# Performance work log

Measured on AMD Instinct MI355X. Metric: run time of the kernel, lower is better.

## Reference

```python
import jax, jax.numpy as jnp
import numpy as np

N, E, IN, HID, ADIM, EDIM, H = 20000, 320000, 128, 128, 16, 16, 2


def _lin(key, out_d, in_d, scale=0.05):
    kw, kb = jax.random.split(key)
    W = jax.random.normal(kw, (out_d, in_d), jnp.float32) * scale
    b = jax.random.normal(kb, (out_d,), jnp.float32) * scale
    return W, b


def _gat_params(key):
    k = jax.random.split(key, 4)
    Wl, bl = _lin(k[0], H * HID, HID)
    Wr, br = _lin(k[1], H * HID, HID)
    We = jax.random.normal(k[2], (H * HID, EDIM), jnp.float32) * 0.05  # lin_edge, no bias
    att = jax.random.normal(k[3], (1, H, HID), jnp.float32) * 0.05
    bias = jnp.zeros((HID,), jnp.float32)  # concat=False -> out bias of size HID
    return Wl, bl, Wr, br, We, att, bias


def setup_inputs() -> dict:
    key = jax.random.key(0)
    ks = jax.random.split(key, 16)
    inp = {}
    inp['x'] = jax.random.normal(ks[0], (N, IN), jnp.float32)
    inp['edge_index'] = jax.random.randint(ks[1], (2, E), 0, N, jnp.int64 if jax.config.jax_enable_x64 else jnp.int32)
    inp['edge_attr'] = jax.random.normal(ks[2], (E, EDIM), jnp.float32)
    inp['action'] = jax.random.normal(ks[3], (N, ADIM), jnp.float32)
    inp['inp_W'], inp['inp_b'] = _lin(ks[4], HID, IN)
    for i, name in enumerate(['s1', 's2', 'sa']):
        Wl, bl, Wr, br, We, att, bias = _gat_params(ks[5 + i])
        inp[f'{name}_Wl'], inp[f'{name}_bl'] = Wl, bl
        inp[f'{name}_Wr'], inp[f'{name}_br'] = Wr, br
        inp[f'{name}_We'], inp[f'{name}_att'], inp[f'{name}_bias'] = We, att, bias
    inp['ap_W'], inp['ap_b'] = _lin(ks[8], HID, ADIM)
    inp['g_W'], inp['g_b'] = _lin(ks[9], HID, HID)
    inp['be_W'], inp['be_b'] = _lin(ks[10], HID, HID)
    inp['q1_W'], inp['q1_b'] = _lin(ks[11], HID, HID)
    inp['q2_W'], inp['q2_b'] = _lin(ks[12], 1, HID)
    return inp


def gatv2(h, src, dst, ea, Wl, bl, Wr, br, We, att, bias):
    """PyG GATv2Conv, heads=H, concat=False (mean over heads), with edge_attr."""
    n = h.shape[0]
    xl = (h @ Wl.T + bl).reshape(n, H, HID)   # source transform
    xr = (h @ Wr.T + br).reshape(n, H, HID)   # destination transform
    em = (ea @ We.T).reshape(-1, H, HID)      # [E,H,C]
    m = jax.nn.leaky_relu(xl[src] + xr[dst] + em, 0.2)   # [E,H,C]
    logit = (m * att).sum(-1)                 # [E,H]
    lmax = jax.ops.segment_max(logit, dst, num_segments=n)
    w = jnp.exp(logit - lmax[dst])
    den = jax.ops.segment_sum(w, dst, num_segments=n)
    alpha = w / den[dst]                      # segment softmax over incoming edges
    out = jax.ops.segment_sum(alpha[..., None] * xl[src], dst, num_segments=n)  # [n,H,C]
    return out.mean(axis=1) + bias


def reference(x, edge_index, edge_attr, action, inp_W, inp_b,
              s1_Wl, s1_bl, s1_Wr, s1_br, s1_We, s1_att, s1_bias,
              s2_Wl, s2_bl, s2_Wr, s2_br, s2_We, s2_att, s2_bias,
              sa_Wl, sa_bl, sa_Wr, sa_br, sa_We, sa_att, sa_bias,
              ap_W, ap_b, g_W, g_b, be_W, be_b, q1_W, q1_b, q2_W, q2_b):
    src, dst = edge_index[0], edge_index[1]
    h = jax.nn.relu(x @ inp_W.T + inp_b)
    h = jax.nn.relu(gatv2(h, src, dst, edge_attr, s1_Wl, s1_bl, s1_Wr, s1_br, s1_We, s1_att, s1_bias))
    h = jax.nn.relu(gatv2(h, src, dst, edge_attr, s2_Wl, s2_bl, s2_Wr, s2_br, s2_We, s2_att, s2_bias))
    a = jax.nn.relu(action @ ap_W.T + ap_b)
    h = (a @ g_W.T + g_b) * h + (a @ be_W.T + be_b)   # FiLM modulation
    h = jax.nn.relu(gatv2(h, src, dst, edge_attr, sa_Wl, sa_bl, sa_Wr, sa_br, sa_We, sa_att, sa_bias))
    h = jax.nn.relu(h @ q1_W.T + q1_b)
    q_node = h @ q2_W.T + q2_b                         # [N,1]
    return q_node.mean(axis=0, keepdims=True)          # [1,1]
```

## Files before the change

### kernel.cpp

```cpp
#include <hip/hip_runtime.h>
#include <hip/hip_bf16.h>


typedef __attribute__((ext_vector_type(8))) short bf16x8;
typedef __attribute__((ext_vector_type(4))) float f32x4;
typedef __attribute__((ext_vector_type(2))) float f32x2;

#define ZERO8 ((bf16x8){0, 0, 0, 0, 0, 0, 0, 0})

__device__ __forceinline__ unsigned short f2bf(float f) {
    union { float f; unsigned int i; } v; v.f = f;
    unsigned int x = v.i;
    x += 0x7fffu + ((x >> 16) & 1u);
    return (unsigned short)(x >> 16);
}
__device__ __forceinline__ unsigned char f2fp8(float f) {
    return (unsigned char)(__builtin_amdgcn_cvt_pk_fp8_f32(f, f, 0, false) & 0xFF);
}
__device__ __forceinline__ void wave_lds_fence() {
    __builtin_amdgcn_wave_barrier();
    asm volatile("s_waitcnt lgkmcnt(0)" ::: "memory");
    __builtin_amdgcn_wave_barrier();
}

#define MAXCVT 16
struct CvtDescs {
    const float* src[MAXCVT];
    unsigned short* dst[MAXCVT];
    int off4[MAXCVT + 1];
    int cnt;
    int* deg; int ndeg4;
    int* ctr; float* col;
};
__global__ __launch_bounds__(256) void cvt_many_kernel(CvtDescs d) {
    const int tid = blockIdx.x * blockDim.x + threadIdx.x;
    const int stride = gridDim.x * blockDim.x;
    const int total = d.off4[d.cnt];
    for (int i = tid; i < total; i += stride) {
        int e = 0;
        while (d.off4[e + 1] <= i) ++e;
        const int j = i - d.off4[e];
        float4 v = ((const float4*)d.src[e])[j];
        ((ushort4*)d.dst[e])[j] = make_ushort4(f2bf(v.x), f2bf(v.y), f2bf(v.z), f2bf(v.w));
    }
    for (int i = tid; i < d.ndeg4; i += stride)
        ((int4*)d.deg)[i] = make_int4(0, 0, 0, 0);
    if (tid == 0) { *d.ctr = 0; *d.col = 0.f; }
}

__global__ void hist_kernel(const int* __restrict__ dst, int* __restrict__ deg, int n) {
    int i = blockIdx.x * blockDim.x + threadIdx.x;
    if (i < n) atomicAdd(&deg[dst[i]], 1);
}

__global__ __launch_bounds__(1024) void scan_kernel(const int* __restrict__ deg,
                                                    int* __restrict__ rowp,
                                                    int* __restrict__ cur, int n) {
    __shared__ int sums[1024];
    const int t = threadIdx.x;
    const int PER = 20;
    int base = t * PER;
    int local[PER];
    int run = 0;
#pragma unroll
    for (int i = 0; i < PER; ++i) {
        int v = (base + i < n) ? deg[base + i] : 0;
        local[i] = run; run += v;
    }
    sums[t] = run; __syncthreads();
    for (int off = 1; off < 1024; off <<= 1) {
        int v = (t >= off) ? sums[t - off] : 0;
        __syncthreads();
        sums[t] += v;
        __syncthreads();
    }
    int offs = (t > 0) ? sums[t - 1] : 0;
#pragma unroll
    for (int i = 0; i < PER; ++i) {
        int idx = base + i;
        if (idx < n) { int v = offs + local[i]; rowp[idx] = v; cur[idx] = v; }
    }
    if (t == 0) rowp[n] = sums[1023];
}

__global__ void scatter_kernel(const int* __restrict__ src, const int* __restrict__ dst,
                               int* __restrict__ cur, const float4* __restrict__ ea,
                               int* __restrict__ csrs,
                               ushort4* __restrict__ eacsr, int n) {
    int i = blockIdx.x * blockDim.x + threadIdx.x;
    if (i < n) {
        int d = dst[i];
        int p = atomicAdd(&cur[d], 1);
        csrs[p] = src[i];
        const float4* er = ea + (size_t)i * 4;
        ushort4* eo = eacsr + (size_t)p * 4;
#pragma unroll
        for (int q = 0; q < 4; ++q) {
            float4 v = er[q];
            eo[q] = make_ushort4(f2bf(v.x), f2bf(v.y), f2bf(v.z), f2bf(v.w));
        }
    }
}

template <bool RELU, bool SPLIT, bool AF32>
__global__ __launch_bounds__(256) void gemm_mfma_kernel(
    const void* __restrict__ Ap, const unsigned short* __restrict__ W,
    const float* __restrict__ bias0, const float* __restrict__ bias1, int bsplit,
    unsigned short* __restrict__ Cbf, unsigned char* __restrict__ Cf8,
    int M, int N, int K) {
    __shared__ unsigned char ctile[SPLIT ? 128 * 64 : 64];
    const int t = threadIdx.x;
    const int wave = t >> 6, lane = t & 63;
    const int lo = lane & 15, quad = lane >> 4;
    const int m0 = blockIdx.y * 128 + wave * 32;
    const int n0 = blockIdx.x * 64;

    f32x4 acc[2][4];
#pragma unroll
    for (int i = 0; i < 2; ++i)
#pragma unroll
        for (int j = 0; j < 4; ++j) acc[i][j] = (f32x4){0.f, 0.f, 0.f, 0.f};

    for (int k0 = 0; k0 < K; k0 += 32) {
        bf16x8 af[2], bfr[4];
#pragma unroll
        for (int mi = 0; mi < 2; ++mi) {
            const int mb = m0 + mi * 16;
            if (mb >= M) { af[mi] = ZERO8; continue; }
            if (AF32) {
                const float* A = (const float*)Ap;
                float4 a0 = *(const float4*)(A + (size_t)(mb + lo) * K + k0 + quad * 8);
                float4 a1 = *(const float4*)(A + (size_t)(mb + lo) * K + k0 + quad * 8 + 4);
                bf16x8 f;
                f[0] = (short)f2bf(a0.x); f[1] = (short)f2bf(a0.y);
                f[2] = (short)f2bf(a0.z); f[3] = (short)f2bf(a0.w);
                f[4] = (short)f2bf(a1.x); f[5] = (short)f2bf(a1.y);
                f[6] = (short)f2bf(a1.z); f[7] = (short)f2bf(a1.w);
                af[mi] = f;
            } else {
                const unsigned short* A = (const unsigned short*)Ap;
                af[mi] = *(const bf16x8*)(A + (size_t)(mb + lo) * K + k0 + quad * 8);
            }
        }
#pragma unroll
        for (int ni = 0; ni < 4; ++ni)
            bfr[ni] = *(const bf16x8*)(W + (size_t)(n0 + ni * 16 + lo) * K + k0 + quad * 8);
#pragma unroll
        for (int mi = 0; mi < 2; ++mi)
#pragma unroll
            for (int ni = 0; ni < 4; ++ni)
                acc[mi][ni] = __builtin_amdgcn_mfma_f32_16x16x32_bf16(af[mi], bfr[ni], acc[mi][ni], 0, 0, 0);
    }

    float bn[4];
#pragma unroll
    for (int ni = 0; ni < 4; ++ni) {
        const int n = n0 + ni * 16 + lo;
        const float* bp = (n < bsplit) ? bias0 : bias1;
        const int bi = (n < bsplit) ? n : n - bsplit;
        bn[ni] = bp[bi];
    }
    if (SPLIT) {
#pragma unroll
        for (int mi = 0; mi < 2; ++mi) {
#pragma unroll
            for (int ni = 0; ni < 4; ++ni) {
                const int n = ni * 16 + lo;
#pragma unroll
                for (int r = 0; r < 4; ++r) {
                    float o = acc[mi][ni][r] + bn[ni];
                    if (RELU) o = fmaxf(o, 0.f);
                    ctile[(wave * 32 + mi * 16 + quad * 4 + r) * 64 + n] = f2fp8(o);
                }
            }
        }
        __syncthreads();
        const int row = t >> 1, half = t & 1;
        const int grow = blockIdx.y * 128 + row;
        if (grow < M) {
            const unsigned char* srcp = &ctile[row * 64 + half * 32];
            unsigned char* dstp = Cf8 + (size_t)grow * 512 + n0 + half * 32;
            *(int4*)(dstp) = *(const int4*)(srcp);
            *(int4*)(dstp + 16) = *(const int4*)(srcp + 16);
        }
    } else {
#pragma unroll
        for (int mi = 0; mi < 2; ++mi) {
            const int mb = m0 + mi * 16;
            if (mb >= M) continue;
#pragma unroll
            for (int ni = 0; ni < 4; ++ni) {
                const int n = n0 + ni * 16 + lo;
#pragma unroll
                for (int r = 0; r < 4; ++r) {
                    float o = acc[mi][ni][r] + bn[ni];
                    if (RELU) o = fmaxf(o, 0.f);
                    Cbf[(size_t)(mb + quad * 4 + r) * N + n] = f2bf(o);
                }
            }
        }
    }
}

__global__ __launch_bounds__(256) void gemm_film_kernel(
    const unsigned short* __restrict__ A, const unsigned short* __restrict__ Wg,
    const unsigned short* __restrict__ Wb, const float* __restrict__ gb,
    const float* __restrict__ bb, unsigned short* __restrict__ hbf, int M) {
    const int K = 128, N = 128;
    const int t = threadIdx.x;
    const int wave = t >> 6, lane = t & 63;
    const int lo = lane & 15, quad = lane >> 4;
    const int m0 = blockIdx.y * 128 + wave * 32;
    const int n0 = blockIdx.x * 64;

    f32x4 accg[2][4], accb[2][4];
#pragma unroll
    for (int i = 0; i < 2; ++i)
#pragma unroll
        for (int j = 0; j < 4; ++j) { accg[i][j] = (f32x4){0.f,0.f,0.f,0.f}; accb[i][j] = accg[i][j]; }

    for (int k0 = 0; k0 < 128; k0 += 32) {
        bf16x8 af[2], bg4[4];
#pragma unroll
        for (int mi = 0; mi < 2; ++mi) {
            const int mb = m0 + mi * 16;
            af[mi] = (mb < M) ? *(const bf16x8*)(A + (size_t)(mb + lo) * K + k0 + quad * 8)
                              : ZERO8;
        }
#pragma unroll
        for (int ni = 0; ni < 4; ++ni)
            bg4[ni] = *(const bf16x8*)(Wg + (size_t)(n0 + ni * 16 + lo) * K + k0 + quad * 8);
#pragma unroll
        for (int mi = 0; mi < 2; ++mi)
#pragma unroll
            for (int ni = 0; ni < 4; ++ni)
                accg[mi][ni] = __builtin_amdgcn_mfma_f32_16x16x32_bf16(af[mi], bg4[ni], accg[mi][ni], 0, 0, 0);
#pragma unroll
        for (int ni = 0; ni < 4; ++ni)
            bg4[ni] = *(const bf16x8*)(Wb + (size_t)(n0 + ni * 16 + lo) * K + k0 + quad * 8);
#pragma unroll
        for (int mi = 0; mi < 2; ++mi)
#pragma unroll
            for (int ni = 0; ni < 4; ++ni)
                accb[mi][ni] = __builtin_amdgcn_mfma_f32_16x16x32_bf16(af[mi], bg4[ni], accb[mi][ni], 0, 0, 0);
    }

#pragma unroll
    for (int mi = 0; mi < 2; ++mi) {
        const int mb = m0 + mi * 16;
        if (mb >= M) continue;
#pragma unroll
        for (int ni = 0; ni < 4; ++ni) {
            const int n = n0 + ni * 16 + lo;
            const float g = gb[n], b = bb[n];
#pragma unroll
            for (int r = 0; r < 4; ++r) {
                const size_t idx = (size_t)(mb + quad * 4 + r) * N + n;
                union { unsigned int i; float f; } hv; hv.i = (unsigned int)hbf[idx] << 16;
                hbf[idx] = f2bf((accg[mi][ni][r] + g) * hv.f + (accb[mi][ni][r] + b));
            }
        }
    }
}

__global__ __launch_bounds__(256) void gemm_q1_kernel(
    const unsigned short* __restrict__ A, const unsigned short* __restrict__ W,
    const float* __restrict__ q1b, const float* __restrict__ q2w,
    const float* __restrict__ q2b, float* __restrict__ outsum,
    float* __restrict__ outv, int* __restrict__ ctr,
    int M, int nblk, float invn) {
    const int K = 128;
    const int t = threadIdx.x;
    const int wave = t >> 6, lane = t & 63;
    const int lo = lane & 15, quad = lane >> 4;
    const int m0 = blockIdx.y * 128 + wave * 32;
    const int n0 = blockIdx.x * 64;
    __shared__ float red[4];

    f32x4 acc[2][4];
#pragma unroll
    for (int i = 0; i < 2; ++i)
#pragma unroll
        for (int j = 0; j < 4; ++j) acc[i][j] = (f32x4){0.f, 0.f, 0.f, 0.f};

    for (int k0 = 0; k0 < K; k0 += 32) {
        bf16x8 af[2], bfr[4];
#pragma unroll
        for (int mi = 0; mi < 2; ++mi) {
            const int mb = m0 + mi * 16;
            af[mi] = (mb < M) ? *(const bf16x8*)(A + (size_t)(mb + lo) * K + k0 + quad * 8)
                              : ZERO8;
        }
#pragma unroll
        for (int ni = 0; ni < 4; ++ni)
            bfr[ni] = *(const bf16x8*)(W + (size_t)(n0 + ni * 16 + lo) * K + k0 + quad * 8);
#pragma unroll
        for (int mi = 0; mi < 2; ++mi)
#pragma unroll
            for (int ni = 0; ni < 4; ++ni)
                acc[mi][ni] = __builtin_amdgcn_mfma_f32_16x16x32_bf16(af[mi], bfr[ni], acc[mi][ni], 0, 0, 0);
    }

    float partial = 0.f;
#pragma unroll
    for (int mi = 0; mi < 2; ++mi) {
        const int mb = m0 + mi * 16;
        if (mb >= M) continue;
#pragma unroll
        for (int ni = 0; ni < 4; ++ni) {
            const int n = n0 + ni * 16 + lo;
            const float b = q1b[n], w = q2w[n];
#pragma unroll
            for (int r = 0; r < 4; ++r)
                partial += fmaxf(acc[mi][ni][r] + b, 0.f) * w;
        }
    }
    partial += __shfl_xor(partial, 1);  partial += __shfl_xor(partial, 2);
    partial += __shfl_xor(partial, 4);  partial += __shfl_xor(partial, 8);
    partial += __shfl_xor(partial, 16); partial += __shfl_xor(partial, 32);
    if (lane == 0) red[wave] = partial;
    __syncthreads();
    if (t == 0) {
        atomicAdd(outsum, red[0] + red[1] + red[2] + red[3]);
        __threadfence();
        unsigned int d = atomicAdd((unsigned int*)ctr, 1u);
        if (d == (unsigned int)(nblk - 1)) {
            float s = atomicAdd(outsum, 0.f);
            outv[0] = s * invn + q2b[0];
        }
    }
}

template <int BK, bool RELU>
__global__ __launch_bounds__(256) void gemm_kernel(const float* __restrict__ A,
                                                   const float* __restrict__ W,
                                                   const float* __restrict__ bp,
                                                   unsigned short* __restrict__ Cbf,
                                                   int M, int N, int K) {
    __shared__ float As[BK][68];
    __shared__ float Ws[BK][68];
    const int t = threadIdx.x;
    const int m0 = blockIdx.y * 64;
    const int n0 = blockIdx.x * 64;
    const int tx = t & 15, ty = t >> 4;
    float acc[4][4];
#pragma unroll
    for (int i = 0; i < 4; ++i)
#pragma unroll
        for (int j = 0; j < 4; ++j) acc[i][j] = 0.f;

    for (int k0 = 0; k0 < K; k0 += BK) {
        const int r = t >> 2, cc = (t & 3) * 4;
        const int arow = m0 + r;
        float4 av = (arow < M) ? *(const float4*)(A + (size_t)arow * K + k0 + cc)
                               : make_float4(0.f, 0.f, 0.f, 0.f);
        As[cc + 0][r] = av.x; As[cc + 1][r] = av.y;
        As[cc + 2][r] = av.z; As[cc + 3][r] = av.w;
        float4 wv = *(const float4*)(W + (size_t)(n0 + r) * K + k0 + cc);
        Ws[cc + 0][r] = wv.x; Ws[cc + 1][r] = wv.y;
        Ws[cc + 2][r] = wv.z; Ws[cc + 3][r] = wv.w;
        __syncthreads();
#pragma unroll
        for (int k = 0; k < BK; ++k) {
            float4 a4 = *(const float4*)&As[k][ty * 4];
            float4 b4 = *(const float4*)&Ws[k][tx * 4];
            float a_[4] = {a4.x, a4.y, a4.z, a4.w};
            float b_[4] = {b4.x, b4.y, b4.z, b4.w};
#pragma unroll
            for (int i = 0; i < 4; ++i)
#pragma unroll
                for (int j = 0; j < 4; ++j) acc[i][j] += a_[i] * b_[j];
        }
        __syncthreads();
    }
    float4 bj = *(const float4*)(bp + n0 + tx * 4);
    float bb[4] = {bj.x, bj.y, bj.z, bj.w};
#pragma unroll
    for (int i = 0; i < 4; ++i) {
        int row = m0 + ty * 4 + i;
        if (row < M) {
            float o[4];
#pragma unroll
            for (int j = 0; j < 4; ++j) {
                o[j] = acc[i][j] + bb[j];
                if (RELU) o[j] = fmaxf(o[j], 0.f);
            }
            *(ushort4*)(Cbf + (size_t)row * N + n0 + tx * 4) =
                make_ushort4(f2bf(o[0]), f2bf(o[1]), f2bf(o[2]), f2bf(o[3]));
        }
    }
}

#define LSTR 272
__global__ __launch_bounds__(256, 4) void gat_fused_kernel(
    const unsigned char* __restrict__ xf8,
    const int* __restrict__ rowp, const int* __restrict__ csrs,
    const unsigned short* __restrict__ eacsr, const unsigned short* __restrict__ we16,
    const float* __restrict__ att, const float* __restrict__ bias,
    unsigned short* __restrict__ houtb, int nnodes) {
    __shared__ float attl[256];
    __shared__ __align__(16) unsigned char xls[4][16 * LSTR];
    __shared__ __align__(16) unsigned char xrs[4][256];
    __shared__ float wls[4][2][16];
    const int tid = threadIdx.x;
    attl[tid] = att[tid];
    const int wave = tid >> 6, lane = tid & 63;
    const int lo = lane & 15, quad = lane >> 4;
    const int sr_row = lane >> 2, c16 = (lane & 3) * 16;

    bf16x8 wef[16];
#pragma unroll
    for (int t = 0; t < 16; ++t)
        wef[t] = (quad < 2) ? *(const bf16x8*)(we16 + (size_t)(t * 16 + lo) * 16 + quad * 8)
                            : ZERO8;
    __syncthreads();

    const int node = blockIdx.x * 4 + wave;
    if (node >= nnodes) return;
    const int rs = rowp[node], re = rowp[node + 1];

    *(unsigned int*)&xrs[wave][4 * lane] =
        *(const unsigned int*)(xf8 + (size_t)node * 512 + 256 + 4 * lane);

    const int h = lane >> 5;
    float den = 0.f;
    float4 acc = make_float4(0.f, 0.f, 0.f, 0.f);

    for (int cb = rs; cb < re; cb += 16) {
        {
            const int pr = min(cb + sr_row, re - 1);
            const int sr = csrs[pr];
            const unsigned char* xs = xf8 + (size_t)sr * 512 + c16;
            unsigned char* ld = &xls[wave][sr_row * LSTR + c16];
#pragma unroll
            for (int j = 0; j < 4; ++j)
                *(int4*)(ld + j * 64) = *(const int4*)(xs + j * 64);
        }
        wave_lds_fence();
        {
            const bool valid = (cb + lo) < re;
            const int p = valid ? (cb + lo) : (re - 1);
            const bf16x8 eaf = (quad < 2)
                ? *(const bf16x8*)(eacsr + (size_t)p * 16 + quad * 8) : ZERO8;
            float ph0 = 0.f, ph1 = 0.f;
#pragma unroll
            for (int t = 0; t < 16; ++t) {
                f32x4 D = __builtin_amdgcn_mfma_f32_16x16x32_bf16(
                    wef[t], eaf, (f32x4){0.f, 0.f, 0.f, 0.f}, 0, 0, 0);
                const int c0 = t * 16 + quad * 4;
                const unsigned int xlu = *(const unsigned int*)&xls[wave][lo * LSTR + c0];
                const unsigned int xru = *(const unsigned int*)&xrs[wave][c0];
                const f32x2 l01 = __builtin_amdgcn_cvt_pk_f32_fp8(xlu, false);
                const f32x2 l23 = __builtin_amdgcn_cvt_pk_f32_fp8(xlu, true);
                const f32x2 r01 = __builtin_amdgcn_cvt_pk_f32_fp8(xru, false);
                const f32x2 r23 = __builtin_amdgcn_cvt_pk_f32_fp8(xru, true);
                const float4 at4 = *(const float4*)&attl[c0];
                float vx = l01.x + r01.x + D[0];
                float vy = l01.y + r01.y + D[1];
                float vz = l23.x + r23.x + D[2];
                float vw = l23.y + r23.y + D[3];
                vx = fmaxf(vx, 0.2f * vx); vy = fmaxf(vy, 0.2f * vy);
                vz = fmaxf(vz, 0.2f * vz); vw = fmaxf(vw, 0.2f * vw);
                const float pt = vx * at4.x + vy * at4.y + vz * at4.z + vw * at4.w;
                if (t < 8) ph0 += pt; else ph1 += pt;
            }
            ph0 += __shfl_xor(ph0, 16); ph0 += __shfl_xor(ph0, 32);
            ph1 += __shfl_xor(ph1, 16); ph1 += __shfl_xor(ph1, 32);
            if (quad == 0) {
                wls[wave][0][lo] = valid ? __expf(fminf(ph0, 60.f)) : 0.f;
                wls[wave][1][lo] = valid ? __expf(fminf(ph1, 60.f)) : 0.f;
            }
        }
        wave_lds_fence();
        {
            const int ne = min(16, re - cb);
            for (int e = 0; e < ne; ++e) {
                const float w = wls[wave][h][e];
                const unsigned int u = *(const unsigned int*)&xls[wave][e * LSTR + 4 * lane];
                const f32x2 p01 = __builtin_amdgcn_cvt_pk_f32_fp8(u, false);
                const f32x2 p23 = __builtin_amdgcn_cvt_pk_f32_fp8(u, true);
                den += w;
                acc.x += w * p01.x; acc.y += w * p01.y;
                acc.z += w * p23.x; acc.w += w * p23.y;
            }
        }
        wave_lds_fence();
    }

    const float inv = (re > rs) ? 1.f / den : 0.f;
    float ox = acc.x * inv, oy = acc.y * inv, oz = acc.z * inv, ow = acc.w * inv;
    ox += __shfl_xor(ox, 32); oy += __shfl_xor(oy, 32);
    oz += __shfl_xor(oz, 32); ow += __shfl_xor(ow, 32);
    if (lane < 32) {
        float4 bu = *(const float4*)(bias + 4 * lane);
        *(ushort4*)(houtb + (size_t)node * 128 + 4 * lane) = make_ushort4(
            f2bf(fmaxf(0.5f * ox + bu.x, 0.f)), f2bf(fmaxf(0.5f * oy + bu.y, 0.f)),
            f2bf(fmaxf(0.5f * oz + bu.z, 0.f)), f2bf(fmaxf(0.5f * ow + bu.w, 0.f)));
    }
}

extern "C" void kernel_launch(void* const* d_in, const int* in_sizes, int n_in,
                              void* d_out, int out_size, void* d_ws, size_t ws_size,
                              hipStream_t stream) {
    const int N = in_sizes[0] / 128;
    const int E = in_sizes[1] / 2;

    typedef const float* fp;
    fp x      = (fp)d_in[0];
    const int* ei = (const int*)d_in[1];
    fp ea     = (fp)d_in[2];
    fp action = (fp)d_in[3];
    fp inp_W  = (fp)d_in[4];
    fp inp_b  = (fp)d_in[5];
    fp ap_W = (fp)d_in[27], ap_b = (fp)d_in[28];
    fp g_W  = (fp)d_in[29], g_b  = (fp)d_in[30];
    fp be_W = (fp)d_in[31], be_b = (fp)d_in[32];
    fp q1_W = (fp)d_in[33], q1_b = (fp)d_in[34];
    fp q2_W = (fp)d_in[35], q2_b = (fp)d_in[36];

    char* base = (char*)d_ws;
    size_t off = 0;
    auto alloc = [&](size_t bytes) { char* p = base + off; off = (off + bytes + 255) & ~(size_t)255; return p; };
    unsigned char*  xf8 = (unsigned char*)alloc((size_t)N * 512);
    float* col  = (float*)alloc(128 * 4);
    int* ctr    = (int*)alloc(256);
    int* deg    = (int*)alloc((size_t)N * 4);
    int* rowp   = (int*)alloc((size_t)(N + 1) * 4);
    int* cur    = (int*)alloc((size_t)N * 4);
    int* csrs   = (int*)alloc((size_t)E * 4);
    unsigned short* eacsr = (unsigned short*)alloc((size_t)E * 16 * 2);
    unsigned short* hbf = (unsigned short*)alloc((size_t)N * 128 * 2);
    unsigned short* abf = (unsigned short*)alloc((size_t)N * 128 * 2);
    unsigned short* wbf = (unsigned short*)alloc((262144 + 3 * 4096) * 2);
    (void)ws_size; (void)n_in; (void)out_size;

    unsigned short* winp = wbf;
    unsigned short* w1l  = wbf + 16384;
    unsigned short* w1r  = w1l + 32768;
    unsigned short* w2l  = w1r + 32768;
    unsigned short* w2r  = w2l + 32768;
    unsigned short* wal  = w2r + 32768;
    unsigned short* war  = wal + 32768;
    unsigned short* wg   = war + 32768;
    unsigned short* wbe  = wg + 16384;
    unsigned short* wq1  = wbe + 16384;
    unsigned short* wep1 = wq1 + 16384;
    unsigned short* wep2 = wep1 + 4096;
    unsigned short* wep3 = wep2 + 4096;

    const int* src = ei;
    const int* dst = ei + E;

    CvtDescs cd;
    int ce = 0, acc4 = 0;
    auto addc = [&](const float* s, unsigned short* d, int n) {
        cd.src[ce] = s; cd.dst[ce] = d; cd.off4[ce] = acc4; acc4 += n / 4; ++ce; };
    addc(inp_W, winp, 16384);
    addc((fp)d_in[6],  w1l, 32768); addc((fp)d_in[8],  w1r, 32768);
    addc((fp)d_in[13], w2l, 32768); addc((fp)d_in[15], w2r, 32768);
    addc((fp)d_in[20], wal, 32768); addc((fp)d_in[22], war, 32768);
    addc(g_W, wg, 16384); addc(be_W, wbe, 16384); addc(q1_W, wq1, 16384);
    addc((fp)d_in[10], wep1, 4096); addc((fp)d_in[17], wep2, 4096); addc((fp)d_in[24], wep3, 4096);
    cd.off4[ce] = acc4; cd.cnt = ce;
    cd.deg = deg; cd.ndeg4 = (N + 3) / 4;
    cd.ctr = ctr; cd.col = col;
    cvt_many_kernel<<<(acc4 + 255) / 256, 256, 0, stream>>>(cd);

    hist_kernel<<<(E + 255) / 256, 256, 0, stream>>>(dst, deg, E);
    scan_kernel<<<1, 1024, 0, stream>>>(deg, rowp, cur, N);
    scatter_kernel<<<(E + 255) / 256, 256, 0, stream>>>(src, dst, cur, (const float4*)ea,
                                                        csrs, (ushort4*)eacsr, E);

    const int my = (N + 127) / 128;
    const int nodeg = (N + 3) / 4;

    auto run_gat = [&](const unsigned short* wep, const float* at, const float* bi,
                       unsigned short* hb) {
        gat_fused_kernel<<<nodeg, 256, 0, stream>>>(xf8, rowp, csrs, eacsr, wep, at, bi, hb, N);
    };

    gemm_mfma_kernel<true, false, true><<<dim3(2, my), 256, 0, stream>>>(
        x, winp, inp_b, inp_b, 128, hbf, nullptr, N, 128, 128);

    gemm_mfma_kernel<false, true, false><<<dim3(8, my), 256, 0, stream>>>(
        hbf, w1l, (fp)d_in[7], (fp)d_in[9], 256, nullptr, xf8, N, 512, 128);
    run_gat(wep1, (fp)d_in[11], (fp)d_in[12], hbf);
    gemm_mfma_kernel<false, true, false><<<dim3(8, my), 256, 0, stream>>>(
        hbf, w2l, (fp)d_in[14], (fp)d_in[16], 256, nullptr, xf8, N, 512, 128);
    run_gat(wep2, (fp)d_in[18], (fp)d_in[19], hbf);

    gemm_kernel<16, true><<<dim3(2, (N + 63) / 64), 256, 0, stream>>>(
        action, ap_W, ap_b, abf, N, 128, 16);
    gemm_film_kernel<<<dim3(2, my), 256, 0, stream>>>(abf, wg, wbe, g_b, be_b, hbf, N);

    gemm_mfma_kernel<false, true, false><<<dim3(8, my), 256, 0, stream>>>(
        hbf, wal, (fp)d_in[21], (fp)d_in[23], 256, nullptr, xf8, N, 512, 128);
    run_gat(wep3, (fp)d_in[25], (fp)d_in[26], hbf);

    gemm_q1_kernel<<<dim3(2, my), 256, 0, stream>>>(
        hbf, wq1, q1_b, q2_W, q2_b, col, (float*)d_out, ctr, N, 2 * my, 1.0f / (float)N);
}
```

Measured before the change: 436.6 us.

## Double-buffer GAT edge gather with register prefetch and LDS-resident edge weights

The fused GATv2 kernel now prefetches the next 16-edge chunk of source features, edge attributes and CSR indices into registers while the current chunk is computed, using ping-pong LDS buffers so the trailing fence can be dropped. Edge-weight MFMA operands move from 16 persistent registers per lane to a shared LDS copy, and the destination features are pre-converted from fp8 to fp32 in LDS. The aggregation loop is fully unrolled over 16 edges with vectorised weight loads, relying on zero weights for padded edges. Nodes with no incoming edges exit early with the bias-only output. This aims to hide global gather latency and lower register pressure, at the cost of extra LDS traffic and more LDS per block.

```diff
diff --git a/kernel.cpp b/kernel.cpp
--- a/kernel.cpp
+++ b/kernel.cpp
@@ -399,66 +399,109 @@
     const float* __restrict__ att, const float* __restrict__ bias,
     unsigned short* __restrict__ houtb, int nnodes) {
     __shared__ float attl[256];
-    __shared__ __align__(16) unsigned char xls[4][16 * LSTR];
-    __shared__ __align__(16) unsigned char xrs[4][256];
-    __shared__ float wls[4][2][16];
+    __shared__ __align__(16) unsigned short wefl[4096];
+    __shared__ __align__(16) unsigned char xls[4][2][16 * LSTR];
+    __shared__ __align__(16) float xrf[4][256];
+    __shared__ float wls[4][2][2][16];
     const int tid = threadIdx.x;
-    attl[tid] = att[tid];
     const int wave = tid >> 6, lane = tid & 63;
     const int lo = lane & 15, quad = lane >> 4;
     const int sr_row = lane >> 2, c16 = (lane & 3) * 16;
 
-    bf16x8 wef[16];
-#pragma unroll
-    for (int t = 0; t < 16; ++t)
-        wef[t] = (quad < 2) ? *(const bf16x8*)(we16 + (size_t)(t * 16 + lo) * 16 + quad * 8)
-                            : ZERO8;
+    attl[tid] = att[tid];
+    {
+        const int4* ws = (const int4*)we16;
+        int4* wd = (int4*)wefl;
+        wd[tid] = ws[tid];
+        wd[tid + 256] = ws[tid + 256];
+    }
+
+    const int node = blockIdx.x * 4 + wave;
+    int rs = 0, re = 0;
+    if (node < nnodes) { rs = rowp[node]; re = rowp[node + 1]; }
+
+    if (node < nnodes) {
+        const unsigned int xru = *(const unsigned int*)(xf8 + (size_t)node * 512 + 256 + 4 * lane);
+        const f32x2 a = __builtin_amdgcn_cvt_pk_f32_fp8(xru, false);
+        const f32x2 b = __builtin_amdgcn_cvt_pk_f32_fp8(xru, true);
+        *(float4*)&xrf[wave][4 * lane] = make_float4(a.x, a.y, b.x, b.y);
+    }
+
     __syncthreads();
 
-    const int node = blockIdx.x * 4 + wave;
     if (node >= nnodes) return;
-    const int rs = rowp[node], re = rowp[node + 1];
-
-    *(unsigned int*)&xrs[wave][4 * lane] =
-        *(const unsigned int*)(xf8 + (size_t)node * 512 + 256 + 4 * lane);
+    if (re <= rs) {
+        if (lane < 32) {
+            float4 bu = *(const float4*)(bias + 4 * lane);
+            *(ushort4*)(houtb + (size_t)node * 128 + 4 * lane) = make_ushort4(
+                f2bf(fmaxf(bu.x, 0.f)), f2bf(fmaxf(bu.y, 0.f)),
+                f2bf(fmaxf(bu.z, 0.f)), f2bf(fmaxf(bu.w, 0.f)));
+        }
+        return;
+    }
 
     const int h = lane >> 5;
     float den = 0.f;
     float4 acc = make_float4(0.f, 0.f, 0.f, 0.f);
 
-    for (int cb = rs; cb < re; cb += 16) {
+    int4 pf0, pf1, pf2, pf3;
+    bf16x8 eaf_pf;
+    int sr_nx;
+    {
+        const int sr0 = csrs[min(rs + sr_row, re - 1)];
+        const unsigned char* xs = xf8 + (size_t)sr0 * 512 + c16;
+        pf0 = *(const int4*)(xs);
+        pf1 = *(const int4*)(xs + 64);
+        pf2 = *(const int4*)(xs + 128);
+        pf3 = *(const int4*)(xs + 192);
+        const int p0 = min(rs + lo, re - 1);
+        eaf_pf = (quad < 2) ? *(const bf16x8*)(eacsr + (size_t)p0 * 16 + quad * 8) : ZERO8;
+        sr_nx = csrs[min(rs + 16 + sr_row, re - 1)];
+    }
+
+    int pb = 0;
+    for (int cb = rs; cb < re; cb += 16, pb ^= 1) {
         {
-            const int pr = min(cb + sr_row, re - 1);
-            const int sr = csrs[pr];
-            const unsigned char* xs = xf8 + (size_t)sr * 512 + c16;
-            unsigned char* ld = &xls[wave][sr_row * LSTR + c16];
-#pragma unroll
-            for (int j = 0; j < 4; ++j)
-                *(int4*)(ld + j * 64) = *(const int4*)(xs + j * 64);
-        }
+            unsigned char* ld = &xls[wave][pb][sr_row * LSTR + c16];
+            *(int4*)(ld)       = pf0;
+            *(int4*)(ld + 64)  = pf1;
+            *(int4*)(ld + 128) = pf2;
+            *(int4*)(ld + 192) = pf3;
+        }
+        const bf16x8 eaf = eaf_pf;
+
+        if (cb + 16 < re) {
+            const unsigned char* xs = xf8 + (size_t)sr_nx * 512 + c16;
+            pf0 = *(const int4*)(xs);
+            pf1 = *(const int4*)(xs + 64);
+            pf2 = *(const int4*)(xs + 128);
+            pf3 = *(const int4*)(xs + 192);
+            const int pn = min(cb + 16 + lo, re - 1);
+            eaf_pf = (quad < 2) ? *(const bf16x8*)(eacsr + (size_t)pn * 16 + quad * 8) : ZERO8;
+            sr_nx = csrs[min(cb + 32 + sr_row, re - 1)];
+        }
+
         wave_lds_fence();
+
         {
             const bool valid = (cb + lo) < re;
-            const int p = valid ? (cb + lo) : (re - 1);
-            const bf16x8 eaf = (quad < 2)
-                ? *(const bf16x8*)(eacsr + (size_t)p * 16 + quad * 8) : ZERO8;
             float ph0 = 0.f, ph1 = 0.f;
 #pragma unroll
             for (int t = 0; t < 16; ++t) {
+                const bf16x8 wf = (quad < 2)
+                    ? *(const bf16x8*)&wefl[(t * 16 + lo) * 16 + quad * 8] : ZERO8;
                 f32x4 D = __builtin_amdgcn_mfma_f32_16x16x32_bf16(
-                    wef[t], eaf, (f32x4){0.f, 0.f, 0.f, 0.f}, 0, 0, 0);
+                    wf, eaf, (f32x4){0.f, 0.f, 0.f, 0.f}, 0, 0, 0);
                 const int c0 = t * 16 + quad * 4;
-                const unsigned int xlu = *(const unsigned int*)&xls[wave][lo * LSTR + c0];
-                const unsigned int xru = *(const unsigned int*)&xrs[wave][c0];
+                const unsigned int xlu = *(const unsigned int*)&xls[wave][pb][lo * LSTR + c0];
                 const f32x2 l01 = __builtin_amdgcn_cvt_pk_f32_fp8(xlu, false);
                 const f32x2 l23 = __builtin_amdgcn_cvt_pk_f32_fp8(xlu, true);
-                const f32x2 r01 = __builtin_amdgcn_cvt_pk_f32_fp8(xru, false);
-                const f32x2 r23 = __builtin_amdgcn_cvt_pk_f32_fp8(xru, true);
+                const float4 xr4 = *(const float4*)&xrf[wave][c0];
                 const float4 at4 = *(const float4*)&attl[c0];
-                float vx = l01.x + r01.x + D[0];
-                float vy = l01.y + r01.y + D[1];
-                float vz = l23.x + r23.x + D[2];
-                float vw = l23.y + r23.y + D[3];
+                float vx = l01.x + xr4.x + D[0];
+                float vy = l01.y + xr4.y + D[1];
+                float vz = l23.x + xr4.z + D[2];
+                float vw = l23.y + xr4.w + D[3];
                 vx = fmaxf(vx, 0.2f * vx); vy = fmaxf(vy, 0.2f * vy);
                 vz = fmaxf(vz, 0.2f * vz); vw = fmaxf(vw, 0.2f * vw);
                 const float pt = vx * at4.x + vy * at4.y + vz * at4.z + vw * at4.w;
@@ -467,16 +510,23 @@
             ph0 += __shfl_xor(ph0, 16); ph0 += __shfl_xor(ph0, 32);
             ph1 += __shfl_xor(ph1, 16); ph1 += __shfl_xor(ph1, 32);
             if (quad == 0) {
-                wls[wave][0][lo] = valid ? __expf(fminf(ph0, 60.f)) : 0.f;
-                wls[wave][1][lo] = valid ? __expf(fminf(ph1, 60.f)) : 0.f;
+                wls[wave][pb][0][lo] = valid ? __expf(fminf(ph0, 60.f)) : 0.f;
+                wls[wave][pb][1][lo] = valid ? __expf(fminf(ph1, 60.f)) : 0.f;
             }
         }
         wave_lds_fence();
+
         {
-            const int ne = min(16, re - cb);
-            for (int e = 0; e < ne; ++e) {
-                const float w = wls[wave][h][e];
-                const unsigned int u = *(const unsigned int*)&xls[wave][e * LSTR + 4 * lane];
+            const float4 w0 = *(const float4*)&wls[wave][pb][h][0];
+            const float4 w1 = *(const float4*)&wls[wave][pb][h][4];
+            const float4 w2 = *(const float4*)&wls[wave][pb][h][8];
+            const float4 w3 = *(const float4*)&wls[wave][pb][h][12];
+            const float wv[16] = {w0.x, w0.y, w0.z, w0.w, w1.x, w1.y, w1.z, w1.w,
+                                  w2.x, w2.y, w2.z, w2.w, w3.x, w3.y, w3.z, w3.w};
+#pragma unroll
+            for (int e = 0; e < 16; ++e) {
+                const float w = wv[e];
+                const unsigned int u = *(const unsigned int*)&xls[wave][pb][e * LSTR + 4 * lane];
                 const f32x2 p01 = __builtin_amdgcn_cvt_pk_f32_fp8(u, false);
                 const f32x2 p23 = __builtin_amdgcn_cvt_pk_f32_fp8(u, true);
                 den += w;
@@ -484,10 +534,9 @@
                 acc.z += w * p23.x; acc.w += w * p23.y;
             }
         }
-        wave_lds_fence();
-    }
-
-    const float inv = (re > rs) ? 1.f / den : 0.f;
+    }
+
+    const float inv = 1.f / den;
     float ox = acc.x * inv, oy = acc.y * inv, oz = acc.z * inv, ow = acc.w * inv;
     ox += __shfl_xor(ox, 32); oy += __shfl_xor(oy, 32);
     oz += __shfl_xor(oz, 32); ow += __shfl_xor(ow, 32);
```

After: 658.0 us. 1.51x slower.
